# Performance work log

Hardware: AMD Instinct MI355X
Metric: run time of the kernel (lower is better)

Reference implementation:

```python
import jax, jax.numpy as jnp
import numpy as np

S, B, C = 7, 2, 20
LAMBDA_COORD = 5.0
LAMBDA_NOOBJ = 0.5
EPS = 1e-6


def _to_abs_xyxy(boxes):
    # boxes: [..., S, S, 4] cell-relative (x,y,w,h) -> normalized image (x1,y1,x2,y2)
    col = jnp.arange(S, dtype=boxes.dtype)            # broadcasts over last grid axis
    row = jnp.arange(S, dtype=boxes.dtype)[:, None]   # broadcasts over second-to-last grid axis
    x, y, w, h = boxes[..., 0], boxes[..., 1], boxes[..., 2], boxes[..., 3]
    cx = (col + x) / S
    cy = (row + y) / S
    return jnp.stack([cx - w / 2, cy - h / 2, cx + w / 2, cy + h / 2], axis=-1)


def _iou(a, b):
    # elementwise IoU of corresponding xyxy boxes (broadcasting allowed)
    x1 = jnp.maximum(a[..., 0], b[..., 0])
    y1 = jnp.maximum(a[..., 1], b[..., 1])
    x2 = jnp.minimum(a[..., 2], b[..., 2])
    y2 = jnp.minimum(a[..., 3], b[..., 3])
    inter = jnp.clip(x2 - x1, 0.0) * jnp.clip(y2 - y1, 0.0)
    area_a = (a[..., 2] - a[..., 0]) * (a[..., 3] - a[..., 1])
    area_b = (b[..., 2] - b[..., 0]) * (b[..., 3] - b[..., 1])
    return inter / (area_a + area_b - inter + EPS)


def setup_inputs() -> dict:
    key = jax.random.key(0)
    kp, kb, kf, kc = jax.random.split(key, 4)
    bs = 16384
    predictions = jax.random.uniform(kp, (bs, S, S, B * 5 + C), dtype=jnp.float32)
    gt_box = jax.random.uniform(kb, (bs, S, S, 4), dtype=jnp.float32)
    obj = (jax.random.uniform(kf, (bs, S, S)) < 0.06).astype(jnp.float32)
    cls = jax.nn.one_hot(jax.random.randint(kc, (bs, S, S), 0, C), C, dtype=jnp.float32)
    targets = jnp.concatenate([gt_box, obj[..., None], cls], axis=-1)
    return {"predictions": predictions, "targets": targets}


def reference(predictions, targets):
    bs = predictions.shape[0]
    pb = predictions[..., : B * 5].reshape(bs, S, S, B, 5)
    boxes = pb[..., :4]                 # [bs,S,S,B,4]
    confs = pb[..., 4]                  # [bs,S,S,B]
    logits = predictions[..., B * 5 :]  # [bs,S,S,C]

    gt_boxes = targets[..., :4]
    objf = (targets[..., 4] > 0).astype(predictions.dtype)  # [bs,S,S]
    gt_cls = targets[..., 5:]

    # IoU per candidate box vs the cell's GT box
    gt_abs = _to_abs_xyxy(gt_boxes)                         # [bs,S,S,4]
    pred_abs = _to_abs_xyxy(jnp.moveaxis(boxes, 3, 1))      # [bs,B,S,S,4]
    ious = jnp.moveaxis(_iou(pred_abs, gt_abs[:, None]), 1, 3)  # [bs,S,S,B]

    best = jnp.argmax(ious, axis=-1)                        # [bs,S,S]
    resp_box = jnp.take_along_axis(boxes, best[..., None, None], axis=3)[..., 0, :]  # [bs,S,S,4]
    resp_conf = jnp.take_along_axis(confs, best[..., None], axis=-1)[..., 0]
    resp_iou = jnp.take_along_axis(ious, best[..., None], axis=-1)[..., 0]

    # Localization loss (masked-sum == torch boolean-mask + sum reduction)
    w = objf[..., None]
    xy_loss = jnp.sum(w * (resp_box[..., :2] - gt_boxes[..., :2]) ** 2)
    wh_loss = jnp.sum(w * (jnp.sqrt(resp_box[..., 2:4] + EPS) - jnp.sqrt(gt_boxes[..., 2:4] + EPS)) ** 2)
    loss_coord = xy_loss + wh_loss

    # Objectness confidence: target is (detached) IoU of responsible box
    loss_conf_obj = jnp.sum(objf * (resp_conf - jax.lax.stop_gradient(resp_iou)) ** 2)

    # No-object confidence: every (cell, box) that is not the responsible box of an object cell
    resp_mask = jax.nn.one_hot(best, B, dtype=predictions.dtype) * objf[..., None]  # [bs,S,S,B]
    loss_conf_noobj = jnp.sum((1.0 - resp_mask) * confs ** 2)

    # Classification: cross-entropy with one-hot GT, summed over object cells
    logp = jax.nn.log_softmax(logits, axis=-1)
    loss_class = -jnp.sum(objf * jnp.sum(gt_cls * logp, axis=-1))

    n = jnp.asarray(bs, predictions.dtype)
    loss_total = (LAMBDA_COORD * loss_coord + loss_conf_obj + LAMBDA_NOOBJ * loss_conf_noobj + loss_class) / n
    # [loss_coord, loss_conf_obj, loss_conf_noobj, loss_class, loss_total]
    return jnp.stack([loss_coord / n, loss_conf_obj / n, loss_conf_noobj / n, loss_class / n, loss_total])
```

## Files before the change

kernel.cpp:

```cpp
#include <hip/hip_runtime.h>
#include <math.h>

namespace {
constexpr int S = 7;
constexpr int B = 2;
constexpr int C = 20;
constexpr int PF = B * 5 + C;
constexpr int TF = 5 + C;
constexpr float EPS = 1e-6f;
constexpr float LAMBDA_COORD = 5.0f;
constexpr float LAMBDA_NOOBJ = 0.5f;
constexpr int BLK = 256;
}

__global__ __launch_bounds__(BLK) void k_main(const float* __restrict__ pred,
                                              const float* __restrict__ tgt,
                                              float* __restrict__ part,
                                              int n_cells) {
    const int tid = threadIdx.x;
    const int cell = blockIdx.x * BLK + tid;

    float v0 = 0.f, v1 = 0.f, v2 = 0.f, v3 = 0.f;
    if (cell < n_cells) {
        const float* p = pred + (size_t)cell * PF;
        const float* t = tgt + (size_t)cell * TF;

        const float2 p45 = *(const float2*)(p + 4);
        const float2 p89 = *(const float2*)(p + 8);
        const float c0 = p45.x, c1 = p89.y;
        const float t4 = t[4];

        v2 = c0 * c0 + c1 * c1;

        if (t4 > 0.f) {
            const int j = cell % S;
            const int i = (cell / S) % S;
            const float invS = 1.0f / (float)S;

            const float2 p01 = *(const float2*)(p + 0);
            const float2 p23 = *(const float2*)(p + 2);
            const float2 p67 = *(const float2*)(p + 6);
            const float gx = t[0], gy = t[1], gw = t[2], gh = t[3];

            const float gcx = ((float)j + gx) * invS;
            const float gcy = ((float)i + gy) * invS;
            const float gx1 = gcx - gw * 0.5f, gy1 = gcy - gh * 0.5f;
            const float gx2 = gcx + gw * 0.5f, gy2 = gcy + gh * 0.5f;
            const float garea = (gx2 - gx1) * (gy2 - gy1);

            const float bx[B]  = {p01.x, p45.y};
            const float by[B]  = {p01.y, p67.x};
            const float bw_[B] = {p23.x, p67.y};
            const float bh[B]  = {p23.y, p89.x};
            const float cf[B]  = {c0, c1};
            float iou[B];
            #pragma unroll
            for (int b = 0; b < B; ++b) {
                const float cx = ((float)j + bx[b]) * invS;
                const float cy = ((float)i + by[b]) * invS;
                const float x1 = cx - bw_[b] * 0.5f, y1 = cy - bh[b] * 0.5f;
                const float x2 = cx + bw_[b] * 0.5f, y2 = cy + bh[b] * 0.5f;
                const float ix1 = fmaxf(x1, gx1), iy1 = fmaxf(y1, gy1);
                const float ix2 = fminf(x2, gx2), iy2 = fminf(y2, gy2);
                const float inter = fmaxf(ix2 - ix1, 0.f) * fmaxf(iy2 - iy1, 0.f);
                const float parea = (x2 - x1) * (y2 - y1);
                iou[b] = inter / (parea + garea - inter + EPS);
            }
            const int best = (iou[1] > iou[0]) ? 1 : 0;
            const float rconf = cf[best], riou = iou[best];

            const float dx = bx[best] - gx, dy = by[best] - gy;
            const float swd = sqrtf(bw_[best] + EPS) - sqrtf(gw + EPS);
            const float shd = sqrtf(bh[best] + EPS) - sqrtf(gh + EPS);
            v0 = dx*dx + dy*dy + swd*swd + shd*shd;
            const float dc = rconf - riou;
            v1 = dc * dc;
            v2 -= rconf * rconf;

            float se = 0.f, dot = 0.f, sg = 0.f;
            #pragma unroll
            for (int c = 0; c < C; c += 2) {
                const float2 lc = *(const float2*)(p + 10 + c);
                const float g0 = t[5 + c], g1 = t[6 + c];
                se  += __expf(lc.x) + __expf(lc.y);
                dot += g0 * lc.x + g1 * lc.y;
                sg  += g0 + g1;
            }
            v3 = __logf(se) * sg - dot;
        }
    }

    float v[4] = {v0, v1, v2, v3};
    #pragma unroll
    for (int off = 32; off >= 1; off >>= 1) {
        v[0] += __shfl_down(v[0], off, 64);
        v[1] += __shfl_down(v[1], off, 64);
        v[2] += __shfl_down(v[2], off, 64);
        v[3] += __shfl_down(v[3], off, 64);
    }
    __shared__ float red[16];
    const int lane = tid & 63;
    const int wave = tid >> 6;
    if (lane == 0) {
        red[wave * 4 + 0] = v[0];
        red[wave * 4 + 1] = v[1];
        red[wave * 4 + 2] = v[2];
        red[wave * 4 + 3] = v[3];
    }
    __syncthreads();
    if (tid < 4)
        part[blockIdx.x * 4 + tid] =
            red[tid] + red[4 + tid] + red[8 + tid] + red[12 + tid];
}

__global__ __launch_bounds__(BLK) void k_fin(const float* __restrict__ part,
                                             float* __restrict__ out,
                                             int nblk, float n) {
    const int tid = threadIdx.x;
    float a0 = 0.f, a1 = 0.f, a2 = 0.f, a3 = 0.f;
    for (int r = tid; r < nblk; r += BLK) {
        const float4 q = *(const float4*)(part + r * 4);
        a0 += q.x; a1 += q.y; a2 += q.z; a3 += q.w;
    }
    float v[4] = {a0, a1, a2, a3};
    #pragma unroll
    for (int off = 32; off >= 1; off >>= 1) {
        v[0] += __shfl_down(v[0], off, 64);
        v[1] += __shfl_down(v[1], off, 64);
        v[2] += __shfl_down(v[2], off, 64);
        v[3] += __shfl_down(v[3], off, 64);
    }
    __shared__ float red[16];
    const int lane = tid & 63;
    const int wave = tid >> 6;
    if (lane == 0) {
        red[wave * 4 + 0] = v[0];
        red[wave * 4 + 1] = v[1];
        red[wave * 4 + 2] = v[2];
        red[wave * 4 + 3] = v[3];
    }
    __syncthreads();
    if (tid == 0) {
        const float coord  = red[0] + red[4] + red[8] + red[12];
        const float cobj   = red[1] + red[5] + red[9] + red[13];
        const float cnoobj = red[2] + red[6] + red[10] + red[14];
        const float ccls   = red[3] + red[7] + red[11] + red[15];
        const float inv = 1.0f / n;
        out[0] = coord * inv;
        out[1] = cobj * inv;
        out[2] = cnoobj * inv;
        out[3] = ccls * inv;
        out[4] = (LAMBDA_COORD * coord + cobj + LAMBDA_NOOBJ * cnoobj + ccls) * inv;
    }
}

extern "C" void kernel_launch(void* const* d_in, const int* in_sizes, int n_in,
                              void* d_out, int out_size, void* d_ws, size_t ws_size,
                              hipStream_t stream) {
    const float* pred = (const float*)d_in[0];
    const float* tgt  = (const float*)d_in[1];
    float* out  = (float*)d_out;
    float* part = (float*)d_ws;

    const int n_cells = in_sizes[0] / PF;
    const float bs = (float)(n_cells / (S * S));
    const int nblk = (n_cells + BLK - 1) / BLK;

    k_main<<<nblk, BLK, 0, stream>>>(pred, tgt, part, n_cells);
    k_fin<<<1, BLK, 0, stream>>>(part, out, nblk, bs);
}
```

Baseline: 201.6 us.

## Stage per-block cell data into LDS with coalesced direct global-to-LDS loads

Each block now cooperatively copies its 256 cells of predictions and targets into shared memory using 16-byte global_load_lds transfers before computing, instead of each thread reading its own strided 120/100-byte records straight from global memory. This makes the global reads fully coalesced and brings in whole cache lines for every cell. The cost is about 56KB of LDS per block, which limits occupancy. The kernel also now always reads the full rows, even though targets beyond the flag were previously read only for object cells, and the strided per-thread LDS reads may hit bank conflicts.

```diff
diff --git a/kernel.cpp b/kernel.cpp
--- a/kernel.cpp
+++ b/kernel.cpp
@@ -11,23 +11,62 @@
 constexpr float LAMBDA_COORD = 5.0f;
 constexpr float LAMBDA_NOOBJ = 0.5f;
 constexpr int BLK = 256;
-}
+constexpr int CH = 256;
+constexpr int PRED_FLOATS = CH * PF;
+constexpr int TGT_FLOATS  = CH * TF;
+}
+
+#define GLOBAL_AS __attribute__((address_space(1)))
+#define LDS_AS    __attribute__((address_space(3)))
 
 __global__ __launch_bounds__(BLK) void k_main(const float* __restrict__ pred,
                                               const float* __restrict__ tgt,
                                               float* __restrict__ part,
                                               int n_cells) {
+    __shared__ float lp[PRED_FLOATS];
+    __shared__ float lt[TGT_FLOATS];
+
     const int tid = threadIdx.x;
-    const int cell = blockIdx.x * BLK + tid;
+    const int block0 = blockIdx.x * CH;
+    const int remc = n_cells - block0;
+    const int cells = remc < CH ? remc : CH;
+
+    const size_t pbase = (size_t)block0 * PF;
+    const size_t tbase = (size_t)block0 * TF;
+
+    if (cells == CH) {
+        #pragma unroll
+        for (int o = 0; o < PRED_FLOATS; o += BLK * 4) {
+            const int idx = o + tid * 4;
+            if (idx < PRED_FLOATS) {
+                __builtin_amdgcn_global_load_lds(
+                    (const GLOBAL_AS void*)(pred + pbase + idx),
+                    (LDS_AS void*)(lp + idx), 16, 0, 0);
+            }
+        }
+        #pragma unroll
+        for (int o = 0; o < TGT_FLOATS; o += BLK * 4) {
+            const int idx = o + tid * 4;
+            if (idx < TGT_FLOATS) {
+                __builtin_amdgcn_global_load_lds(
+                    (const GLOBAL_AS void*)(tgt + tbase + idx),
+                    (LDS_AS void*)(lt + idx), 16, 0, 0);
+            }
+        }
+        asm volatile("s_waitcnt vmcnt(0)" ::: "memory");
+    } else {
+        for (int o = tid; o < cells * PF; o += BLK) lp[o] = pred[pbase + o];
+        for (int o = tid; o < cells * TF; o += BLK) lt[o] = tgt[tbase + o];
+    }
+    __syncthreads();
 
     float v0 = 0.f, v1 = 0.f, v2 = 0.f, v3 = 0.f;
-    if (cell < n_cells) {
-        const float* p = pred + (size_t)cell * PF;
-        const float* t = tgt + (size_t)cell * TF;
-
-        const float2 p45 = *(const float2*)(p + 4);
-        const float2 p89 = *(const float2*)(p + 8);
-        const float c0 = p45.x, c1 = p89.y;
+    if (tid < cells) {
+        const int cell = block0 + tid;
+        const float* p = lp + tid * PF;
+        const float* t = lt + tid * TF;
+
+        const float c0 = p[4], c1 = p[9];
         const float t4 = t[4];
 
         v2 = c0 * c0 + c1 * c1;
@@ -48,10 +87,10 @@
             const float gx2 = gcx + gw * 0.5f, gy2 = gcy + gh * 0.5f;
             const float garea = (gx2 - gx1) * (gy2 - gy1);
 
-            const float bx[B]  = {p01.x, p45.y};
+            const float bx[B]  = {p01.x, p[5]};
             const float by[B]  = {p01.y, p67.x};
             const float bw_[B] = {p23.x, p67.y};
-            const float bh[B]  = {p23.y, p89.x};
+            const float bh[B]  = {p23.y, p[8]};
             const float cf[B]  = {c0, c1};
             float iou[B];
             #pragma unroll
@@ -164,7 +203,7 @@
 
     const int n_cells = in_sizes[0] / PF;
     const float bs = (float)(n_cells / (S * S));
-    const int nblk = (n_cells + BLK - 1) / BLK;
+    const int nblk = (n_cells + CH - 1) / CH;
 
     k_main<<<nblk, BLK, 0, stream>>>(pred, tgt, part, n_cells);
     k_fin<<<1, BLK, 0, stream>>>(part, out, nblk, bs);
```

Result: no change. 198.1 us (-1.7%).

## Stage cell chunks into LDS via async global_load_lds with double buffering

Applied to the files above, without the earlier changes.

Replaces the one-cell-per-thread direct global reads with a persistent grid of 256 blocks. Each block loops over 256-cell chunks and copies them into shared memory with coalesced 16-byte global_load_lds transfers, double-buffered so the next chunk loads while the current one is computed. The goal is fully coalesced streaming of the strided 30-float and 25-float records. The cost is about 113 KB of LDS per block, which limits occupancy to one block per CU. A grid of only 256 blocks may also not fill the GPU well enough to saturate bandwidth.

```diff
diff --git a/kernel.cpp b/kernel.cpp
--- a/kernel.cpp
+++ b/kernel.cpp
@@ -11,83 +11,145 @@
 constexpr float LAMBDA_COORD = 5.0f;
 constexpr float LAMBDA_NOOBJ = 0.5f;
 constexpr int BLK = 256;
+constexpr int CH = 256;
+constexpr int NB = 256;
+constexpr int PREDF = CH * PF;
+constexpr int TGTF  = CH * TF;
+}
+
+#define GLOBAL_AS __attribute__((address_space(1)))
+#define LDS_AS    __attribute__((address_space(3)))
+
+__device__ __forceinline__ void cell_terms(const float* __restrict__ p,
+                                           const float* __restrict__ t,
+                                           int cell,
+                                           float& v0, float& v1, float& v2, float& v3)
+{
+    const float c0 = p[4], c1 = p[9];
+    v2 += c0 * c0 + c1 * c1;
+
+    if (t[4] > 0.f) {
+        const int j = cell % S;
+        const int i = (cell / S) % S;
+        const float invS = 1.0f / (float)S;
+
+        const float2 p01 = *(const float2*)(p + 0);
+        const float2 p23 = *(const float2*)(p + 2);
+        const float2 p67 = *(const float2*)(p + 6);
+        const float gx = t[0], gy = t[1], gw = t[2], gh = t[3];
+
+        const float gcx = ((float)j + gx) * invS;
+        const float gcy = ((float)i + gy) * invS;
+        const float gx1 = gcx - gw * 0.5f, gy1 = gcy - gh * 0.5f;
+        const float gx2 = gcx + gw * 0.5f, gy2 = gcy + gh * 0.5f;
+        const float garea = (gx2 - gx1) * (gy2 - gy1);
+
+        const float bx[B]  = {p01.x, p[5]};
+        const float by[B]  = {p01.y, p67.x};
+        const float bw_[B] = {p23.x, p67.y};
+        const float bh[B]  = {p23.y, p[8]};
+        const float cf[B]  = {c0, c1};
+        float iou[B];
+        #pragma unroll
+        for (int b = 0; b < B; ++b) {
+            const float cx = ((float)j + bx[b]) * invS;
+            const float cy = ((float)i + by[b]) * invS;
+            const float x1 = cx - bw_[b] * 0.5f, y1 = cy - bh[b] * 0.5f;
+            const float x2 = cx + bw_[b] * 0.5f, y2 = cy + bh[b] * 0.5f;
+            const float ix1 = fmaxf(x1, gx1), iy1 = fmaxf(y1, gy1);
+            const float ix2 = fminf(x2, gx2), iy2 = fminf(y2, gy2);
+            const float inter = fmaxf(ix2 - ix1, 0.f) * fmaxf(iy2 - iy1, 0.f);
+            const float parea = (x2 - x1) * (y2 - y1);
+            iou[b] = inter / (parea + garea - inter + EPS);
+        }
+        const int best = (iou[1] > iou[0]) ? 1 : 0;
+        const float rconf = cf[best], riou = iou[best];
+
+        const float dx = bx[best] - gx, dy = by[best] - gy;
+        const float swd = sqrtf(bw_[best] + EPS) - sqrtf(gw + EPS);
+        const float shd = sqrtf(bh[best] + EPS) - sqrtf(gh + EPS);
+        v0 += dx*dx + dy*dy + swd*swd + shd*shd;
+        const float dc = rconf - riou;
+        v1 += dc * dc;
+        v2 -= rconf * rconf;
+
+        float se = 0.f, dot = 0.f, sg = 0.f;
+        #pragma unroll
+        for (int c = 0; c < C; c += 2) {
+            const float2 lc = *(const float2*)(p + 10 + c);
+            const float g0 = t[5 + c], g1 = t[6 + c];
+            se  += __expf(lc.x) + __expf(lc.y);
+            dot += g0 * lc.x + g1 * lc.y;
+            sg  += g0 + g1;
+        }
+        v3 += __logf(se) * sg - dot;
+    }
 }
 
 __global__ __launch_bounds__(BLK) void k_main(const float* __restrict__ pred,
                                               const float* __restrict__ tgt,
                                               float* __restrict__ part,
-                                              int n_cells) {
+                                              int n_cells)
+{
+    __shared__ float lp[2][PREDF];
+    __shared__ float lt[2][TGTF];
+
     const int tid = threadIdx.x;
-    const int cell = blockIdx.x * BLK + tid;
+    const int bid = blockIdx.x;
+    const int t4o = tid * 4;
+    const int nfull = n_cells / CH;
+
+    int m = 0;
+    if (nfull > bid) m = (nfull - bid - 1) / NB + 1;
 
     float v0 = 0.f, v1 = 0.f, v2 = 0.f, v3 = 0.f;
-    if (cell < n_cells) {
-        const float* p = pred + (size_t)cell * PF;
-        const float* t = tgt + (size_t)cell * TF;
-
-        const float2 p45 = *(const float2*)(p + 4);
-        const float2 p89 = *(const float2*)(p + 8);
-        const float c0 = p45.x, c1 = p89.y;
-        const float t4 = t[4];
-
-        v2 = c0 * c0 + c1 * c1;
-
-        if (t4 > 0.f) {
-            const int j = cell % S;
-            const int i = (cell / S) % S;
-            const float invS = 1.0f / (float)S;
-
-            const float2 p01 = *(const float2*)(p + 0);
-            const float2 p23 = *(const float2*)(p + 2);
-            const float2 p67 = *(const float2*)(p + 6);
-            const float gx = t[0], gy = t[1], gw = t[2], gh = t[3];
-
-            const float gcx = ((float)j + gx) * invS;
-            const float gcy = ((float)i + gy) * invS;
-            const float gx1 = gcx - gw * 0.5f, gy1 = gcy - gh * 0.5f;
-            const float gx2 = gcx + gw * 0.5f, gy2 = gcy + gh * 0.5f;
-            const float garea = (gx2 - gx1) * (gy2 - gy1);
-
-            const float bx[B]  = {p01.x, p45.y};
-            const float by[B]  = {p01.y, p67.x};
-            const float bw_[B] = {p23.x, p67.y};
-            const float bh[B]  = {p23.y, p89.x};
-            const float cf[B]  = {c0, c1};
-            float iou[B];
-            #pragma unroll
-            for (int b = 0; b < B; ++b) {
-                const float cx = ((float)j + bx[b]) * invS;
-                const float cy = ((float)i + by[b]) * invS;
-                const float x1 = cx - bw_[b] * 0.5f, y1 = cy - bh[b] * 0.5f;
-                const float x2 = cx + bw_[b] * 0.5f, y2 = cy + bh[b] * 0.5f;
-                const float ix1 = fmaxf(x1, gx1), iy1 = fmaxf(y1, gy1);
-                const float ix2 = fminf(x2, gx2), iy2 = fminf(y2, gy2);
-                const float inter = fmaxf(ix2 - ix1, 0.f) * fmaxf(iy2 - iy1, 0.f);
-                const float parea = (x2 - x1) * (y2 - y1);
-                iou[b] = inter / (parea + garea - inter + EPS);
-            }
-            const int best = (iou[1] > iou[0]) ? 1 : 0;
-            const float rconf = cf[best], riou = iou[best];
-
-            const float dx = bx[best] - gx, dy = by[best] - gy;
-            const float swd = sqrtf(bw_[best] + EPS) - sqrtf(gw + EPS);
-            const float shd = sqrtf(bh[best] + EPS) - sqrtf(gh + EPS);
-            v0 = dx*dx + dy*dy + swd*swd + shd*shd;
-            const float dc = rconf - riou;
-            v1 = dc * dc;
-            v2 -= rconf * rconf;
-
-            float se = 0.f, dot = 0.f, sg = 0.f;
-            #pragma unroll
-            for (int c = 0; c < C; c += 2) {
-                const float2 lc = *(const float2*)(p + 10 + c);
-                const float g0 = t[5 + c], g1 = t[6 + c];
-                se  += __expf(lc.x) + __expf(lc.y);
-                dot += g0 * lc.x + g1 * lc.y;
-                sg  += g0 + g1;
-            }
-            v3 = __logf(se) * sg - dot;
-        }
+
+    auto stage = [&](int buf, int chunk) {
+        const float* ps = pred + (size_t)chunk * PREDF;
+        const float* ts = tgt + (size_t)chunk * TGTF;
+        #pragma unroll
+        for (int s = 0; s < 7; ++s) {
+            __builtin_amdgcn_global_load_lds(
+                (const GLOBAL_AS void*)(ps + s * 1024 + t4o),
+                (LDS_AS void*)(&lp[buf][s * 1024 + t4o]), 16, 0, 0);
+        }
+        if (tid < 128) {
+            __builtin_amdgcn_global_load_lds(
+                (const GLOBAL_AS void*)(ps + 7168 + t4o),
+                (LDS_AS void*)(&lp[buf][7168 + t4o]), 16, 0, 0);
+        }
+        #pragma unroll
+        for (int s = 0; s < 6; ++s) {
+            __builtin_amdgcn_global_load_lds(
+                (const GLOBAL_AS void*)(ts + s * 1024 + t4o),
+                (LDS_AS void*)(&lt[buf][s * 1024 + t4o]), 16, 0, 0);
+        }
+        if (tid < 64) {
+            __builtin_amdgcn_global_load_lds(
+                (const GLOBAL_AS void*)(ts + 6144 + t4o),
+                (LDS_AS void*)(&lt[buf][6144 + t4o]), 16, 0, 0);
+        }
+    };
+
+    if (m > 0) stage(0, bid);
+
+    for (int k = 0; k < m; ++k) {
+        asm volatile("s_waitcnt vmcnt(0)" ::: "memory");
+        __builtin_amdgcn_s_barrier();
+        asm volatile("" ::: "memory");
+        if (k + 1 < m) stage((k + 1) & 1, bid + (k + 1) * NB);
+        const int buf = k & 1;
+        const int cbase = (bid + k * NB) * CH;
+        cell_terms(&lp[buf][tid * PF], &lt[buf][tid * TF], cbase + tid,
+                   v0, v1, v2, v3);
+        asm volatile("" ::: "memory");
+    }
+
+    const int rem = n_cells - nfull * CH;
+    if (rem > 0 && bid == NB - 1 && tid < rem) {
+        const int cell = nfull * CH + tid;
+        cell_terms(pred + (size_t)cell * PF, tgt + (size_t)cell * TF, cell,
+                   v0, v1, v2, v3);
     }
 
     float v[4] = {v0, v1, v2, v3};
@@ -109,7 +171,7 @@
     }
     __syncthreads();
     if (tid < 4)
-        part[blockIdx.x * 4 + tid] =
+        part[bid * 4 + tid] =
             red[tid] + red[4 + tid] + red[8 + tid] + red[12 + tid];
 }
 
@@ -164,8 +226,7 @@
 
     const int n_cells = in_sizes[0] / PF;
     const float bs = (float)(n_cells / (S * S));
-    const int nblk = (n_cells + BLK - 1) / BLK;
-
-    k_main<<<nblk, BLK, 0, stream>>>(pred, tgt, part, n_cells);
-    k_fin<<<1, BLK, 0, stream>>>(part, out, nblk, bs);
-}
+
+    k_main<<<NB, BLK, 0, stream>>>(pred, tgt, part, n_cells);
+    k_fin<<<1, BLK, 0, stream>>>(part, out, NB, bs);
+}
```

New measurement: 200.6 us. Within noise of the previous version (-0.5%).

## Stream cell chunks via async global-to-LDS loads with triple buffering in persistent waves

Applied to the files above, without the earlier changes.

Replaces one-thread-per-cell strided global loads with a persistent grid of single-wave blocks. Each block copies contiguous 32-cell chunks of predictions and targets into LDS using global_load_lds, triple-buffered, with manual vmcnt waits so loads overlap compute. The goal is fully coalesced 16-byte loads and hidden memory latency in place of uncoalesced 120-byte-stride per-thread reads. In exchange only half of each wave computes, it relies on hand-written waitcnt ordering that is fragile, and it uses a fixed grid size of 1792 blocks.

```diff
diff --git a/kernel.cpp b/kernel.cpp
--- a/kernel.cpp
+++ b/kernel.cpp
@@ -10,84 +10,149 @@
 constexpr float EPS = 1e-6f;
 constexpr float LAMBDA_COORD = 5.0f;
 constexpr float LAMBDA_NOOBJ = 0.5f;
-constexpr int BLK = 256;
-}
-
-__global__ __launch_bounds__(BLK) void k_main(const float* __restrict__ pred,
-                                              const float* __restrict__ tgt,
-                                              float* __restrict__ part,
-                                              int n_cells) {
-    const int tid = threadIdx.x;
-    const int cell = blockIdx.x * BLK + tid;
+
+constexpr int WT = 64;
+constexpr int CC = 32;
+constexpr int NBUF = 3;
+constexpr int NBLK = 1792;
+constexpr int PB = CC * PF;
+constexpr int TB = CC * TF;
+}
+
+#define GLOBAL_AS __attribute__((address_space(1)))
+#define LDS_AS    __attribute__((address_space(3)))
+
+__device__ __forceinline__ void cell_terms(const float* __restrict__ p,
+                                           const float* __restrict__ t,
+                                           int cell,
+                                           float& v0, float& v1, float& v2, float& v3)
+{
+    const float c0 = p[4], c1 = p[9];
+    v2 += c0 * c0 + c1 * c1;
+
+    if (t[4] > 0.f) {
+        const int j = cell % S;
+        const int i = (cell / S) % S;
+        const float invS = 1.0f / (float)S;
+
+        const float2 p01 = *(const float2*)(p + 0);
+        const float2 p23 = *(const float2*)(p + 2);
+        const float2 p67 = *(const float2*)(p + 6);
+        const float gx = t[0], gy = t[1], gw = t[2], gh = t[3];
+
+        const float gcx = ((float)j + gx) * invS;
+        const float gcy = ((float)i + gy) * invS;
+        const float gx1 = gcx - gw * 0.5f, gy1 = gcy - gh * 0.5f;
+        const float gx2 = gcx + gw * 0.5f, gy2 = gcy + gh * 0.5f;
+        const float garea = (gx2 - gx1) * (gy2 - gy1);
+
+        const float bx[B]  = {p01.x, p[5]};
+        const float by[B]  = {p01.y, p67.x};
+        const float bw_[B] = {p23.x, p67.y};
+        const float bh[B]  = {p23.y, p[8]};
+        const float cf[B]  = {c0, c1};
+        float iou[B];
+        #pragma unroll
+        for (int b = 0; b < B; ++b) {
+            const float cx = ((float)j + bx[b]) * invS;
+            const float cy = ((float)i + by[b]) * invS;
+            const float x1 = cx - bw_[b] * 0.5f, y1 = cy - bh[b] * 0.5f;
+            const float x2 = cx + bw_[b] * 0.5f, y2 = cy + bh[b] * 0.5f;
+            const float ix1 = fmaxf(x1, gx1), iy1 = fmaxf(y1, gy1);
+            const float ix2 = fminf(x2, gx2), iy2 = fminf(y2, gy2);
+            const float inter = fmaxf(ix2 - ix1, 0.f) * fmaxf(iy2 - iy1, 0.f);
+            const float parea = (x2 - x1) * (y2 - y1);
+            iou[b] = inter / (parea + garea - inter + EPS);
+        }
+        const int best = (iou[1] > iou[0]) ? 1 : 0;
+        const float rconf = cf[best], riou = iou[best];
+
+        const float dx = bx[best] - gx, dy = by[best] - gy;
+        const float swd = sqrtf(bw_[best] + EPS) - sqrtf(gw + EPS);
+        const float shd = sqrtf(bh[best] + EPS) - sqrtf(gh + EPS);
+        v0 += dx*dx + dy*dy + swd*swd + shd*shd;
+        const float dc = rconf - riou;
+        v1 += dc * dc;
+        v2 -= rconf * rconf;
+
+        float se = 0.f, dot = 0.f, sg = 0.f;
+        #pragma unroll
+        for (int c = 0; c < C; c += 2) {
+            const float2 lc = *(const float2*)(p + 10 + c);
+            const float g0 = t[5 + c], g1 = t[6 + c];
+            se  += __expf(lc.x) + __expf(lc.y);
+            dot += g0 * lc.x + g1 * lc.y;
+            sg  += g0 + g1;
+        }
+        v3 += __logf(se) * sg - dot;
+    }
+}
+
+__global__ __launch_bounds__(WT) void k_main(const float* __restrict__ pred,
+                                             const float* __restrict__ tgt,
+                                             float* __restrict__ part,
+                                             int n_cells)
+{
+    __shared__ float lp[NBUF][PB];
+    __shared__ float lt[NBUF][TB];
+
+    const int lane = threadIdx.x;
+    const int bid = blockIdx.x;
+    const int NC = n_cells / CC;
+    const int o4 = lane * 4;
+
+    int m = 0;
+    if (bid < NC) m = (NC - bid - 1) / NBLK + 1;
 
     float v0 = 0.f, v1 = 0.f, v2 = 0.f, v3 = 0.f;
-    if (cell < n_cells) {
-        const float* p = pred + (size_t)cell * PF;
-        const float* t = tgt + (size_t)cell * TF;
-
-        const float2 p45 = *(const float2*)(p + 4);
-        const float2 p89 = *(const float2*)(p + 8);
-        const float c0 = p45.x, c1 = p89.y;
-        const float t4 = t[4];
-
-        v2 = c0 * c0 + c1 * c1;
-
-        if (t4 > 0.f) {
-            const int j = cell % S;
-            const int i = (cell / S) % S;
-            const float invS = 1.0f / (float)S;
-
-            const float2 p01 = *(const float2*)(p + 0);
-            const float2 p23 = *(const float2*)(p + 2);
-            const float2 p67 = *(const float2*)(p + 6);
-            const float gx = t[0], gy = t[1], gw = t[2], gh = t[3];
-
-            const float gcx = ((float)j + gx) * invS;
-            const float gcy = ((float)i + gy) * invS;
-            const float gx1 = gcx - gw * 0.5f, gy1 = gcy - gh * 0.5f;
-            const float gx2 = gcx + gw * 0.5f, gy2 = gcy + gh * 0.5f;
-            const float garea = (gx2 - gx1) * (gy2 - gy1);
-
-            const float bx[B]  = {p01.x, p45.y};
-            const float by[B]  = {p01.y, p67.x};
-            const float bw_[B] = {p23.x, p67.y};
-            const float bh[B]  = {p23.y, p89.x};
-            const float cf[B]  = {c0, c1};
-            float iou[B];
-            #pragma unroll
-            for (int b = 0; b < B; ++b) {
-                const float cx = ((float)j + bx[b]) * invS;
-                const float cy = ((float)i + by[b]) * invS;
-                const float x1 = cx - bw_[b] * 0.5f, y1 = cy - bh[b] * 0.5f;
-                const float x2 = cx + bw_[b] * 0.5f, y2 = cy + bh[b] * 0.5f;
-                const float ix1 = fmaxf(x1, gx1), iy1 = fmaxf(y1, gy1);
-                const float ix2 = fminf(x2, gx2), iy2 = fminf(y2, gy2);
-                const float inter = fmaxf(ix2 - ix1, 0.f) * fmaxf(iy2 - iy1, 0.f);
-                const float parea = (x2 - x1) * (y2 - y1);
-                iou[b] = inter / (parea + garea - inter + EPS);
-            }
-            const int best = (iou[1] > iou[0]) ? 1 : 0;
-            const float rconf = cf[best], riou = iou[best];
-
-            const float dx = bx[best] - gx, dy = by[best] - gy;
-            const float swd = sqrtf(bw_[best] + EPS) - sqrtf(gw + EPS);
-            const float shd = sqrtf(bh[best] + EPS) - sqrtf(gh + EPS);
-            v0 = dx*dx + dy*dy + swd*swd + shd*shd;
-            const float dc = rconf - riou;
-            v1 = dc * dc;
-            v2 -= rconf * rconf;
-
-            float se = 0.f, dot = 0.f, sg = 0.f;
-            #pragma unroll
-            for (int c = 0; c < C; c += 2) {
-                const float2 lc = *(const float2*)(p + 10 + c);
-                const float g0 = t[5 + c], g1 = t[6 + c];
-                se  += __expf(lc.x) + __expf(lc.y);
-                dot += g0 * lc.x + g1 * lc.y;
-                sg  += g0 + g1;
-            }
-            v3 = __logf(se) * sg - dot;
-        }
+
+    auto stage = [&](int buf, int c) {
+        const float* ps = pred + (size_t)c * PB;
+        const float* ts = tgt + (size_t)c * TB;
+        float* dp = &lp[buf][0];
+        float* dt = &lt[buf][0];
+        __builtin_amdgcn_global_load_lds((const GLOBAL_AS void*)(ps + o4),
+                                         (LDS_AS void*)(dp + o4), 16, 0, 0);
+        __builtin_amdgcn_global_load_lds((const GLOBAL_AS void*)(ps + 256 + o4),
+                                         (LDS_AS void*)(dp + 256 + o4), 16, 0, 0);
+        __builtin_amdgcn_global_load_lds((const GLOBAL_AS void*)(ps + 512 + o4),
+                                         (LDS_AS void*)(dp + 512 + o4), 16, 0, 0);
+        __builtin_amdgcn_global_load_lds((const GLOBAL_AS void*)(ps + 704 + o4),
+                                         (LDS_AS void*)(dp + 704 + o4), 16, 0, 0);
+        __builtin_amdgcn_global_load_lds((const GLOBAL_AS void*)(ts + o4),
+                                         (LDS_AS void*)(dt + o4), 16, 0, 0);
+        __builtin_amdgcn_global_load_lds((const GLOBAL_AS void*)(ts + 256 + o4),
+                                         (LDS_AS void*)(dt + 256 + o4), 16, 0, 0);
+        __builtin_amdgcn_global_load_lds((const GLOBAL_AS void*)(ts + 512 + o4),
+                                         (LDS_AS void*)(dt + 512 + o4), 16, 0, 0);
+        __builtin_amdgcn_global_load_lds((const GLOBAL_AS void*)(ts + 544 + o4),
+                                         (LDS_AS void*)(dt + 544 + o4), 16, 0, 0);
+    };
+
+    if (m > 0) stage(0, bid);
+    if (m > 1) stage(1, bid + NBLK);
+    if (m > 2) stage(2, bid + 2 * NBLK);
+
+    for (int k = 0; k < m; ++k) {
+        const int rem = m - 1 - k;
+        if (rem >= 2)      asm volatile("s_waitcnt vmcnt(16)" ::: "memory");
+        else if (rem == 1) asm volatile("s_waitcnt vmcnt(8)" ::: "memory");
+        else               asm volatile("s_waitcnt vmcnt(0)" ::: "memory");
+
+        const int buf = k % NBUF;
+        const int c = bid + k * NBLK;
+        if (lane < CC)
+            cell_terms(&lp[buf][lane * PF], &lt[buf][lane * TF],
+                       c * CC + lane, v0, v1, v2, v3);
+        asm volatile("s_waitcnt lgkmcnt(0)" ::: "memory");
+        if (k + NBUF < m) stage(buf, bid + (k + NBUF) * NBLK);
+    }
+
+    const int remc = n_cells - NC * CC;
+    if (remc > 0 && bid == 0 && lane < remc) {
+        const int cell = NC * CC + lane;
+        cell_terms(pred + (size_t)cell * PF, tgt + (size_t)cell * TF, cell,
+                   v0, v1, v2, v3);
     }
 
     float v[4] = {v0, v1, v2, v3};
@@ -98,27 +163,20 @@
         v[2] += __shfl_down(v[2], off, 64);
         v[3] += __shfl_down(v[3], off, 64);
     }
-    __shared__ float red[16];
-    const int lane = tid & 63;
-    const int wave = tid >> 6;
     if (lane == 0) {
-        red[wave * 4 + 0] = v[0];
-        red[wave * 4 + 1] = v[1];
-        red[wave * 4 + 2] = v[2];
-        red[wave * 4 + 3] = v[3];
-    }
-    __syncthreads();
-    if (tid < 4)
-        part[blockIdx.x * 4 + tid] =
-            red[tid] + red[4 + tid] + red[8 + tid] + red[12 + tid];
-}
-
-__global__ __launch_bounds__(BLK) void k_fin(const float* __restrict__ part,
+        part[bid * 4 + 0] = v[0];
+        part[bid * 4 + 1] = v[1];
+        part[bid * 4 + 2] = v[2];
+        part[bid * 4 + 3] = v[3];
+    }
+}
+
+__global__ __launch_bounds__(256) void k_fin(const float* __restrict__ part,
                                              float* __restrict__ out,
                                              int nblk, float n) {
     const int tid = threadIdx.x;
     float a0 = 0.f, a1 = 0.f, a2 = 0.f, a3 = 0.f;
-    for (int r = tid; r < nblk; r += BLK) {
+    for (int r = tid; r < nblk; r += 256) {
         const float4 q = *(const float4*)(part + r * 4);
         a0 += q.x; a1 += q.y; a2 += q.z; a3 += q.w;
     }
@@ -164,8 +222,7 @@
 
     const int n_cells = in_sizes[0] / PF;
     const float bs = (float)(n_cells / (S * S));
-    const int nblk = (n_cells + BLK - 1) / BLK;
-
-    k_main<<<nblk, BLK, 0, stream>>>(pred, tgt, part, n_cells);
-    k_fin<<<1, BLK, 0, stream>>>(part, out, nblk, bs);
-}
+
+    k_main<<<NBLK, WT, 0, stream>>>(pred, tgt, part, n_cells);
+    k_fin<<<1, 256, 0, stream>>>(part, out, NBLK, bs);
+}
```

After: 201.2 us. No clear change (-0.2%).
